# Optimization experiments

Measured on AMD Instinct MI355X. Metric: run time of the kernel, lower is better.

## Reference

```python
import jax, jax.numpy as jnp
import numpy as np
from jax import lax

B, S, IN, H = 16, 128, 200, 256


def _lstm_dir(x_tb, Wih, Whh, bih, bhh):
    # x_tb: [S, B, in]; PyTorch LSTM gate order (i, f, g, o)
    h0 = jnp.zeros((x_tb.shape[1], H), x_tb.dtype)

    def step(carry, x_t):
        h, c = carry
        g = x_t @ Wih.T + h @ Whh.T + bih + bhh  # [B, 4H]
        i, f, gg, o = jnp.split(g, 4, axis=-1)
        c = jax.nn.sigmoid(f) * c + jax.nn.sigmoid(i) * jnp.tanh(gg)
        h = jax.nn.sigmoid(o) * jnp.tanh(c)
        return (h, c), h

    _, hs = lax.scan(step, (h0, h0), x_tb)
    return hs  # [S, B, H]


def _bilstm_layer(x, Wih, Whh, bih, bhh):
    # x: [B, S, in]; params stacked over direction axis [2, ...]
    xt = jnp.swapaxes(x, 0, 1)
    f = _lstm_dir(xt, Wih[0], Whh[0], bih[0], bhh[0])
    b = _lstm_dir(xt[::-1], Wih[1], Whh[1], bih[1], bhh[1])[::-1]
    return jnp.swapaxes(jnp.concatenate([f, b], axis=-1), 0, 1)  # [B, S, 2H]


def _forward(sentence, Wih0, Whh0, bih0, bhh0, Wih1, Whh1, bih1, bhh1,
             W1, b1, W2, b2, W3, b3, tree):
    emb = _bilstm_layer(sentence, Wih0, Whh0, bih0, bhh0)  # [B,S,512]
    emb = _bilstm_layer(emb, Wih1, Whh1, bih1, bhh1)       # [B,S,512]
    D = emb.shape[-1]
    # fc1 on concat(emb[v1], emb[v2]) == per-node halves + broadcast add
    Ha = emb @ W1[:, :D].T   # [B,S,256] head part
    Hb = emb @ W1[:, D:].T   # [B,S,256] dependent part
    h1 = jax.nn.relu(Ha[:, :, None, :] + Hb[:, None, :, :] + b1)  # [B,S,S,256]
    h2 = jax.nn.relu(h1 @ W2.T + b2)                               # [B,S,S,128]
    score = jax.nn.relu(jnp.squeeze(h2 @ W3.T + b3, -1))           # [B,S,S]
    v = jnp.arange(S)
    # valid edges: dep >= 1, head != dep (root col 0 and diagonal stay 0)
    mask = (v[None, :] != v[:, None]) & (v[None, :] >= 1)
    score = score * mask[None, :, :]

    heads, deps = tree[:, 1:, 0], tree[:, 1:, 1]  # [B, S-1]
    K = S - 1
    idx = jnp.broadcast_to(deps[:, None, :], (B, S, K))
    cols = jnp.take_along_axis(score, idx, axis=2)     # score[b, j, dep_k]
    excl = v[None, :, None] == deps[:, None, :]        # exclude j == dep
    norm = jnp.sum(jnp.where(excl, 0.0, jnp.exp(cols)), axis=1)  # [B,K]
    num = score[jnp.arange(B)[:, None], heads, deps]             # [B,K]
    loss = jnp.sum(jnp.sum(jnp.log(norm) - num, axis=-1) / (S - 1))
    return loss, score


def setup_inputs() -> dict:
    key = jax.random.key(0)
    ks = jax.random.split(key, 17)
    sc = jnp.float32(0.05)

    def n(k, shape):
        return jax.random.normal(k, shape, jnp.float32) * sc

    return {
        "sentence": jax.random.normal(ks[0], (B, S, IN), jnp.float32),
        "Wih0": n(ks[1], (2, 4 * H, IN)),
        "Whh0": n(ks[2], (2, 4 * H, H)),
        "bih0": n(ks[3], (2, 4 * H)),
        "bhh0": n(ks[4], (2, 4 * H)),
        "Wih1": n(ks[5], (2, 4 * H, 2 * H)),
        "Whh1": n(ks[6], (2, 4 * H, H)),
        "bih1": n(ks[7], (2, 4 * H)),
        "bhh1": n(ks[8], (2, 4 * H)),
        "W1": n(ks[9], (256, 1024)),
        "b1": n(ks[10], (256,)),
        "W2": n(ks[11], (128, 256)),
        "b2": n(ks[12], (128,)),
        "W3": n(ks[13], (1, 128)),
        "b3": n(ks[14], (1,)),
        "real_dependency_tree": jax.random.randint(ks[15], (B, S, 2), 0, S, jnp.int32),
        "real_seq_len": jnp.full((B,), S, jnp.int32),
    }


def reference(sentence, Wih0, Whh0, bih0, bhh0, Wih1, Whh1, bih1, bhh1,
              W1, b1, W2, b2, W3, b3, real_dependency_tree, real_seq_len):
    # all sentences are full length S (real_seq_len == S), so shapes are static
    del real_seq_len
    return _forward(sentence, Wih0, Whh0, bih0, bhh0, Wih1, Whh1, bih1, bhh1,
                    W1, b1, W2, b2, W3, b3, real_dependency_tree)
```

## Files before the change

kernel.cpp:

```cpp
#include <hip/hip_runtime.h>
#include <hip/hip_bf16.h>
#include <cstdint>
#include <cstddef>


typedef __attribute__((ext_vector_type(8))) short bf16x8;
typedef __attribute__((ext_vector_type(4))) float f32x4;
typedef __attribute__((ext_vector_type(4))) unsigned short u16x4;

__device__ __forceinline__ float bf2f(unsigned short u) {
    return __uint_as_float(((unsigned)u) << 16);
}
__device__ __forceinline__ unsigned short f2bf(float f) {
    unsigned u = __float_as_uint(f);
    u = (u + 0x7FFFu + ((u >> 16) & 1u)) >> 16;
    return (unsigned short)u;
}

__device__ __forceinline__ unsigned f2e4m3(float f) {
    unsigned u = __float_as_uint(f);
    unsigned s = (u >> 24) & 0x80u;
    int expf_ = (int)((u >> 23) & 0xFF);
    if (expf_ == 0) return s;
    int exp = expf_ - 127;
    if (exp < -10) return s;
    unsigned M = (u & 0x7FFFFF) | 0x800000;
    int e8 = exp + 7;
    int shift = 20;
    if (e8 < 1) { shift = 21 - e8; e8 = 0; }
    unsigned q = M >> shift;
    unsigned rem = M & ((1u << shift) - 1u);
    unsigned half = 1u << (shift - 1);
    if (rem > half || (rem == half && (q & 1))) q++;
    if (q >= 16) { q >>= 1; e8++; }
    if (e8 == 0 && (q & 8)) e8 = 1;
    if (e8 >= 16 || (e8 == 15 && (q & 7) == 7)) return s | 0x7Eu;
    return s | ((unsigned)e8 << 4) | (q & 7u);
}


__global__ void k_transpose_N1024(const float* __restrict__ src, float* __restrict__ dst, int K) {
    int z = blockIdx.z;
    int idx = blockIdx.x * 256 + threadIdx.x;
    if (idx >= K * 1024) return;
    int k = idx >> 10, n = idx & 1023;
    dst[(size_t)z * K * 1024 + idx] = src[(size_t)z * 1024 * K + (size_t)n * K + k];
}

__global__ void k_wfrag8(const float* __restrict__ Whh, unsigned char* __restrict__ Wfrag8) {
    int idx = blockIdx.x * 256 + threadIdx.x;
    int l = idx & 63;
    int t = (idx >> 6) & 3;
    int ks = (idx >> 8) & 7;
    int w = (idx >> 11) & 15;
    int d = idx >> 15;
    int r = l & 15;
    int kbase = ks * 32 + (l >> 4) * 8;
    int row = (r & 3) * 256 + w * 16 + t * 4 + (r >> 2);
    const float* src = Whh + (size_t)d * (1024 * 256) + (size_t)row * 256 + kbase;
    unsigned char* dst = Wfrag8 + (size_t)idx * 8;
#pragma unroll
    for (int e = 0; e < 8; ++e) {
        int c = (e & 1) * 4 + (e >> 1);
        dst[e] = (unsigned char)f2e4m3(64.f * src[c]);
    }
}

__global__ void k_w2frag(const float* __restrict__ W2, unsigned short* __restrict__ w2f) {
    int idx = blockIdx.x * 256 + threadIdx.x;
    if (idx >= 4096) return;
    int l = idx & 63;
    int ks = (idx >> 6) & 7;
    int nt = idx >> 9;
    const float* src = W2 + (size_t)(nt * 16 + (l & 15)) * 256 + ks * 32 + (l >> 4) * 8;
    unsigned short* dst = w2f + (size_t)idx * 8;
#pragma unroll
    for (int e = 0; e < 8; ++e) dst[e] = f2bf(src[e]);
}

__global__ void k_w1t(const float* __restrict__ W1, float* __restrict__ dst) {
    int idx = blockIdx.x * 256 + threadIdx.x;
    if (idx >= 512 * 512) return;
    int k = idx >> 9, o = idx & 511;
    dst[idx] = (o < 256) ? W1[(size_t)o * 1024 + k] : W1[(size_t)(o - 256) * 1024 + 512 + k];
}

__global__ void k_bias(const float* __restrict__ bih0, const float* __restrict__ bhh0,
                       const float* __restrict__ bih1, const float* __restrict__ bhh1,
                       const float* __restrict__ b1,
                       float* __restrict__ bsum0, float* __restrict__ bsum1, float* __restrict__ bhab) {
    int idx = blockIdx.x * 256 + threadIdx.x;
    if (idx < 2048) bsum0[idx] = bih0[idx] + bhh0[idx];
    else if (idx < 4096) { int i = idx - 2048; bsum1[i] = bih1[i] + bhh1[i]; }
    else if (idx < 4608) { int i = idx - 4096; bhab[i] = (i < 256) ? b1[i] : 0.f; }
}

__global__ __launch_bounds__(256) void k_reorder(const float* __restrict__ xg, float* __restrict__ xgf) {
    int idx = blockIdx.x * 256 + threadIdx.x;
    int n4 = idx & 255;
    int m = (idx >> 8) & 2047;
    int d = idx >> 19;
    int n0 = n4 * 4;
    int q = n0 >> 8;
    int jbase = n0 & 255;
    int b = m >> 7, t = m & 127;
    float4 v = *(const float4*)(xg + ((size_t)(d * 2048 + m)) * 1024 + n0);
    float* base = xgf + (size_t)d * 2097152;
    float vv[4] = {v.x * 64.f, v.y * 64.f, v.z * 64.f, v.w * 64.f};
#pragma unroll
    for (int dj = 0; dj < 4; ++dj) {
        int j = jbase + dj;
        int fi = (t * 4096 + (j >> 4) * 256 + ((j >> 2) & 3) * 64 + dj * 16 + b) * 4 + q;
        base[fi] = vv[dj];
    }
}

__global__ __launch_bounds__(256) void k_gemm(
    const float* __restrict__ A, const float* __restrict__ Wt,
    const float* __restrict__ bias, float* __restrict__ out,
    int M, int K, int N)
{
    int z = blockIdx.z;
    const float* Wtz = Wt + (size_t)z * K * N;
    float* outz = out + (size_t)z * M * N;
    const float* biasz = bias + (size_t)z * N;

    __shared__ float As[16 * 512];
    int tid = threadIdx.x;
    int mq = tid >> 6;
    int nq = tid & 63;
    int n0 = blockIdx.x * 256 + nq * 4;
    int mbase = blockIdx.y * 16;

    for (int r = 0; r < 16; ++r) {
        const float* Ar = A + (size_t)(mbase + r) * K;
        for (int c = tid; c < K; c += 256) As[r * K + c] = Ar[c];
    }
    __syncthreads();

    float4 bv = *(const float4*)(biasz + n0);
    float acc[4][4];
#pragma unroll
    for (int mi = 0; mi < 4; mi++) { acc[mi][0] = bv.x; acc[mi][1] = bv.y; acc[mi][2] = bv.z; acc[mi][3] = bv.w; }

    const float* asr = As + (mq * 4) * K;
    for (int k = 0; k < K; ++k) {
        float4 w = *(const float4*)(Wtz + (size_t)k * N + n0);
        float x0 = asr[k];
        float x1 = asr[K + k];
        float x2 = asr[2 * K + k];
        float x3 = asr[3 * K + k];
        acc[0][0] += x0 * w.x; acc[0][1] += x0 * w.y; acc[0][2] += x0 * w.z; acc[0][3] += x0 * w.w;
        acc[1][0] += x1 * w.x; acc[1][1] += x1 * w.y; acc[1][2] += x1 * w.z; acc[1][3] += x1 * w.w;
        acc[2][0] += x2 * w.x; acc[2][1] += x2 * w.y; acc[2][2] += x2 * w.z; acc[2][3] += x2 * w.w;
        acc[3][0] += x3 * w.x; acc[3][1] += x3 * w.y; acc[3][2] += x3 * w.z; acc[3][3] += x3 * w.w;
    }
#pragma unroll
    for (int mi = 0; mi < 4; mi++) {
        size_t m = (size_t)mbase + mq * 4 + mi;
        *(float4*)(outz + m * N + n0) = make_float4(acc[mi][0], acc[mi][1], acc[mi][2], acc[mi][3]);
    }
}

__global__ __launch_bounds__(256) void k_gemm_tl(
    const unsigned short* __restrict__ embt, const float* __restrict__ Wt,
    const float* __restrict__ bias, float* __restrict__ out,
    int K, int N)
{
    int z = blockIdx.z;
    const float* Wtz = Wt + (size_t)z * K * N;
    float* outz = out + (size_t)z * 2048 * N;
    const float* biasz = bias + (size_t)z * N;

    __shared__ float As[16 * 512];
    int tid = threadIdx.x;
    int mq = tid >> 6;
    int nq = tid & 63;
    int n0 = blockIdx.x * 256 + nq * 4;
    int mbase = blockIdx.y * 16;
    int bb = mbase >> 7;
    int tt0 = mbase & 127;

    for (int r = 0; r < 16; ++r) {
        const unsigned short* Ar = embt + (size_t)(tt0 + r) * 8192 + bb;
        for (int c = tid; c < K; c += 256) As[r * K + c] = bf2f(Ar[c * 16]);
    }
    __syncthreads();

    float4 bv = *(const float4*)(biasz + n0);
    float acc[4][4];
#pragma unroll
    for (int mi = 0; mi < 4; mi++) { acc[mi][0] = bv.x; acc[mi][1] = bv.y; acc[mi][2] = bv.z; acc[mi][3] = bv.w; }

    const float* asr = As + (mq * 4) * K;
    for (int k = 0; k < K; ++k) {
        float4 w = *(const float4*)(Wtz + (size_t)k * N + n0);
        float x0 = asr[k];
        float x1 = asr[K + k];
        float x2 = asr[2 * K + k];
        float x3 = asr[3 * K + k];
        acc[0][0] += x0 * w.x; acc[0][1] += x0 * w.y; acc[0][2] += x0 * w.z; acc[0][3] += x0 * w.w;
        acc[1][0] += x1 * w.x; acc[1][1] += x1 * w.y; acc[1][2] += x1 * w.z; acc[1][3] += x1 * w.w;
        acc[2][0] += x2 * w.x; acc[2][1] += x2 * w.y; acc[2][2] += x2 * w.z; acc[2][3] += x2 * w.w;
        acc[3][0] += x3 * w.x; acc[3][1] += x3 * w.y; acc[3][2] += x3 * w.z; acc[3][3] += x3 * w.w;
    }
#pragma unroll
    for (int mi = 0; mi < 4; mi++) {
        size_t m = (size_t)mbase + mq * 4 + mi;
        *(float4*)(outz + m * N + n0) = make_float4(acc[mi][0], acc[mi][1], acc[mi][2], acc[mi][3]);
    }
}

#define GATE8(A, C, H) { \
    float gi = A[0] * 0.015625f, gf = A[1] * 0.015625f, gg = A[2] * 0.015625f, go = A[3] * 0.015625f; \
    float si = __builtin_amdgcn_rcpf(1.f + __expf(-gi)); \
    float sf = __builtin_amdgcn_rcpf(1.f + __expf(-gf)); \
    float so = __builtin_amdgcn_rcpf(1.f + __expf(-go)); \
    float eg = __expf(2.f * gg); \
    float tg = 1.f - 2.f * __builtin_amdgcn_rcpf(eg + 1.f); \
    C = sf * C + si * tg; \
    float ec = __expf(2.f * C); \
    float tc = 1.f - 2.f * __builtin_amdgcn_rcpf(ec + 1.f); \
    H = so * tc; }

__global__ __launch_bounds__(512, 2) void k_lstm_mfma(
    const float* __restrict__ xgf,
    const unsigned char* __restrict__ Wfrag8,
    unsigned short* __restrict__ embt)
{
    const int d = blockIdx.x;
    const int tid = threadIdx.x;
    const int wv = tid >> 6;
    const int l = tid & 63;
    const int b = l & 15;
    const int jh = l >> 4;
    const int s0 = wv * 2, s1 = wv * 2 + 1;

    __shared__ __align__(8) unsigned char hB[4096];

    const unsigned char* wg0 = Wfrag8 + ((size_t)(d * 16 + s0)) * 16384;
    const unsigned char* wg1 = Wfrag8 + ((size_t)(d * 16 + s1)) * 16384;
    long W0[8][4], W1[8][4];
#pragma unroll
    for (int ks = 0; ks < 8; ++ks)
#pragma unroll
        for (int t4 = 0; t4 < 4; ++t4) {
            W0[ks][t4] = *(const long*)(wg0 + ((size_t)((ks * 4 + t4) * 64 + l)) * 8);
            W1[ks][t4] = *(const long*)(wg1 + ((size_t)((ks * 4 + t4) * 64 + l)) * 8);
        }
#pragma unroll
    for (int ks = 0; ks < 8; ++ks)
#pragma unroll
        for (int t4 = 0; t4 < 4; ++t4) {
            asm volatile("" : "+v"(W0[ks][t4]));
            asm volatile("" : "+v"(W1[ks][t4]));
        }

    ((uint64_t*)hB)[tid] = 0ull;

    const int sgn = d ? -1 : 1;
    int t = d ? 127 : 0;
    const f32x4* xb = (const f32x4*)(xgf) + (size_t)d * 524288;
    const int xo0 = s0 * 256 + l;
    const int xo1 = s1 * 256 + l;

    f32x4 a0 = xb[t * 4096 + xo0];
    f32x4 a1 = xb[t * 4096 + xo0 + 64];
    f32x4 a2 = xb[t * 4096 + xo0 + 128];
    f32x4 a3 = xb[t * 4096 + xo0 + 192];
    f32x4 e0 = xb[t * 4096 + xo1];
    f32x4 e1 = xb[t * 4096 + xo1 + 64];
    f32x4 e2 = xb[t * 4096 + xo1 + 128];
    f32x4 e3 = xb[t * 4096 + xo1 + 192];

    float c0 = 0.f, c1 = 0.f, c2 = 0.f, c3 = 0.f;
    float c4 = 0.f, c5 = 0.f, c6 = 0.f, c7 = 0.f;
    const int hrd = jh * 128 + b * 8;
    unsigned short* ep0 = embt + (size_t)d * 4096 + (size_t)s0 * 256 + l;
    unsigned short* ep1 = embt + (size_t)d * 4096 + (size_t)s1 * 256 + l;
    unsigned char* hw0 = hB + s0 * 256 + b * 8 + jh * 2;
    unsigned char* hw1 = hB + s1 * 256 + b * 8 + jh * 2;
    __syncthreads();

    for (int s = 0; s < 128; ++s) {
#pragma unroll
        for (int ks = 0; ks < 8; ++ks) {
            long hf = *(const long*)(hB + ks * 512 + hrd);
            a0 = __builtin_amdgcn_mfma_f32_16x16x32_fp8_fp8(W0[ks][0], hf, a0, 0, 0, 0);
            a1 = __builtin_amdgcn_mfma_f32_16x16x32_fp8_fp8(W0[ks][1], hf, a1, 0, 0, 0);
            a2 = __builtin_amdgcn_mfma_f32_16x16x32_fp8_fp8(W0[ks][2], hf, a2, 0, 0, 0);
            a3 = __builtin_amdgcn_mfma_f32_16x16x32_fp8_fp8(W0[ks][3], hf, a3, 0, 0, 0);
            e0 = __builtin_amdgcn_mfma_f32_16x16x32_fp8_fp8(W1[ks][0], hf, e0, 0, 0, 0);
            e1 = __builtin_amdgcn_mfma_f32_16x16x32_fp8_fp8(W1[ks][1], hf, e1, 0, 0, 0);
            e2 = __builtin_amdgcn_mfma_f32_16x16x32_fp8_fp8(W1[ks][2], hf, e2, 0, 0, 0);
            e3 = __builtin_amdgcn_mfma_f32_16x16x32_fp8_fp8(W1[ks][3], hf, e3, 0, 0, 0);
        }

        float h0, h1, h2, h3, h4, h5, h6, h7;
        GATE8(a0, c0, h0);
        GATE8(a1, c1, h1);
        GATE8(a2, c2, h2);
        GATE8(a3, c3, h3);
        GATE8(e0, c4, h4);
        GATE8(e1, c5, h5);
        GATE8(e2, c6, h6);
        GATE8(e3, c7, h7);

        unsigned r01, r23, r45, r67;
        asm("v_cvt_pk_bf16_f32 %0, %1, %2" : "=v"(r01) : "v"(h0), "v"(h1));
        asm("v_cvt_pk_bf16_f32 %0, %1, %2" : "=v"(r23) : "v"(h2), "v"(h3));
        asm("v_cvt_pk_bf16_f32 %0, %1, %2" : "=v"(r45) : "v"(h4), "v"(h5));
        asm("v_cvt_pk_bf16_f32 %0, %1, %2" : "=v"(r67) : "v"(h6), "v"(h7));
        {
            unsigned short* p0 = ep0 + (size_t)t * 8192;
            p0[0]   = (unsigned short)r01;
            p0[64]  = (unsigned short)(r01 >> 16);
            p0[128] = (unsigned short)r23;
            p0[192] = (unsigned short)(r23 >> 16);
            unsigned short* p1 = ep1 + (size_t)t * 8192;
            p1[0]   = (unsigned short)r45;
            p1[64]  = (unsigned short)(r45 >> 16);
            p1[128] = (unsigned short)r67;
            p1[192] = (unsigned short)(r67 >> 16);
        }

        unsigned q01 = __builtin_amdgcn_cvt_pk_fp8_f32(h0, h1, 0, false);
        unsigned q23 = __builtin_amdgcn_cvt_pk_fp8_f32(h2, h3, 0, false);
        unsigned q45 = __builtin_amdgcn_cvt_pk_fp8_f32(h4, h5, 0, false);
        unsigned q67 = __builtin_amdgcn_cvt_pk_fp8_f32(h6, h7, 0, false);

        int tn = (s == 127) ? t : (t + sgn);
        a0 = xb[tn * 4096 + xo0];
        a1 = xb[tn * 4096 + xo0 + 64];
        a2 = xb[tn * 4096 + xo0 + 128];
        a3 = xb[tn * 4096 + xo0 + 192];
        e0 = xb[tn * 4096 + xo1];
        e1 = xb[tn * 4096 + xo1 + 64];
        e2 = xb[tn * 4096 + xo1 + 128];
        e3 = xb[tn * 4096 + xo1 + 192];
        __syncthreads();
        *(unsigned short*)(hw0)       = (unsigned short)q01;
        *(unsigned short*)(hw0 + 128) = (unsigned short)q23;
        *(unsigned short*)(hw1)       = (unsigned short)q45;
        *(unsigned short*)(hw1 + 128) = (unsigned short)q67;
        __syncthreads();
        t = tn;
    }
}

__global__ __launch_bounds__(256, 2) void k_scorer_mfma(
    const float* __restrict__ HaHb, const unsigned short* __restrict__ w2f,
    const float* __restrict__ b2, const float* __restrict__ W3,
    const float* __restrict__ b3v, float* __restrict__ score)
{
    const int jt = blockIdx.x, it = blockIdx.y, b = blockIdx.z;
    const int j0 = jt * 16, i0 = it * 16;
    const int tid = threadIdx.x;
    const int w = tid >> 6;
    const int l = tid & 63;
    const int n_l = l & 15;
    const int kq = l >> 4;

    __shared__ __align__(16) unsigned short HaS[16 * 264];
    __shared__ __align__(16) unsigned short HbS[16 * 264];

    {
        const float* base = HaHb + ((size_t)(b * 128)) * 512;
        int rr = tid >> 4;
        int q = tid & 15;
#pragma unroll
        for (int rep = 0; rep < 4; ++rep) {
            int k0 = q * 4 + rep * 64;
            float4 va = *(const float4*)(base + (size_t)(i0 + rr) * 512 + k0);
            float4 vb = *(const float4*)(base + (size_t)(j0 + rr) * 512 + 256 + k0);
            u16x4 ua = { f2bf(va.x), f2bf(va.y), f2bf(va.z), f2bf(va.w) };
            u16x4 ub = { f2bf(vb.x), f2bf(vb.y), f2bf(vb.z), f2bf(vb.w) };
            *(u16x4*)(&HaS[rr * 264 + k0]) = ua;
            *(u16x4*)(&HbS[rr * 264 + k0]) = ub;
        }
    }

    float b2v[8], w3v[8];
#pragma unroll
    for (int nt = 0; nt < 8; ++nt) {
        b2v[nt] = b2[nt * 16 + n_l];
        w3v[nt] = W3[nt * 16 + n_l];
    }

    f32x4 acc[4][8];
#pragma unroll
    for (int il = 0; il < 4; ++il)
#pragma unroll
        for (int nt = 0; nt < 8; ++nt) acc[il][nt] = f32x4{0.f, 0.f, 0.f, 0.f};

    const bf16x8* wbase = (const bf16x8*)w2f;
    bf16x8 wf[8], wfn[8];
#pragma unroll
    for (int nt = 0; nt < 8; ++nt) wf[nt] = wbase[(nt * 8 + 0) * 64 + l];

    __syncthreads();

#pragma unroll
    for (int ks = 0; ks < 8; ++ks) {
        if (ks < 7) {
#pragma unroll
            for (int nt = 0; nt < 8; ++nt) wfn[nt] = wbase[(nt * 8 + ks + 1) * 64 + l];
        }
#pragma unroll
        for (int il = 0; il < 4; ++il) {
            const int irow = w * 4 + il;
            bf16x8 ha = *(const bf16x8*)(&HaS[irow * 264 + ks * 32 + kq * 8]);
            bf16x8 hb = *(const bf16x8*)(&HbS[n_l * 264 + ks * 32 + kq * 8]);
            bf16x8 av;
#pragma unroll
            for (int e = 0; e < 8; ++e) {
                float v = bf2f((unsigned short)ha[e]) + bf2f((unsigned short)hb[e]);
                v = v > 0.f ? v : 0.f;
                av[e] = (short)f2bf(v);
            }
#pragma unroll
            for (int nt = 0; nt < 8; ++nt)
                acc[il][nt] = __builtin_amdgcn_mfma_f32_16x16x32_bf16(av, wf[nt], acc[il][nt], 0, 0, 0);
        }
#pragma unroll
        for (int nt = 0; nt < 8; ++nt) wf[nt] = wfn[nt];
    }

    const float bb3 = b3v[0];
#pragma unroll
    for (int il = 0; il < 4; ++il) {
        float p[4];
#pragma unroll
        for (int reg = 0; reg < 4; ++reg) {
            float v = 0.f;
#pragma unroll
            for (int nt = 0; nt < 8; ++nt) {
                float h2v = acc[il][nt][reg] + b2v[nt];
                h2v = h2v > 0.f ? h2v : 0.f;
                v += h2v * w3v[nt];
            }
            p[reg] = v;
        }
#pragma unroll
        for (int m = 1; m < 16; m <<= 1) {
            p[0] += __shfl_xor(p[0], m);
            p[1] += __shfl_xor(p[1], m);
            p[2] += __shfl_xor(p[2], m);
            p[3] += __shfl_xor(p[3], m);
        }
        if (n_l == 0) {
            const int i = i0 + w * 4 + il;
            const int jb = j0 + kq * 4;
            float4 sv;
            float* pv = &sv.x;
#pragma unroll
            for (int reg = 0; reg < 4; ++reg) {
                int jg = jb + reg;
                float sc = p[reg] + bb3;
                sc = sc > 0.f ? sc : 0.f;
                if (jg == i || jg == 0) sc = 0.f;
                pv[reg] = sc;
            }
            *(float4*)(&score[((size_t)(b * 128 + i)) * 128 + jb]) = sv;
        }
    }
}

__global__ __launch_bounds__(128) void k_loss1(
    const float* __restrict__ score, const int* __restrict__ tree, float* __restrict__ res)
{
    int k = blockIdx.x;
    int b = blockIdx.y;
    int head = tree[((size_t)b * 128 + k + 1) * 2 + 0];
    int dep  = tree[((size_t)b * 128 + k + 1) * 2 + 1];
    int i = threadIdx.x;
    float s = score[((size_t)b * 128 + i) * 128 + dep];
    float v = (i == dep) ? 0.f : __expf(s);
    __shared__ float redu[2];
#pragma unroll
    for (int off = 32; off >= 1; off >>= 1) v += __shfl_down(v, off, 64);
    if ((i & 63) == 0) redu[i >> 6] = v;
    __syncthreads();
    if (i == 0) {
        float norm = redu[0] + redu[1];
        float num = score[((size_t)b * 128 + head) * 128 + dep];
        res[b * 127 + k] = __logf(norm) - num;
    }
}

__global__ __launch_bounds__(256) void k_loss2(const float* __restrict__ res, float* __restrict__ out) {
    int tid = threadIdx.x;
    float a = 0.f;
    for (int idx = tid; idx < 16 * 127; idx += 256) a += res[idx];
    __shared__ float sm[256];
    sm[tid] = a;
    __syncthreads();
    for (int off = 128; off >= 1; off >>= 1) {
        if (tid < off) sm[tid] += sm[tid + off];
        __syncthreads();
    }
    if (tid == 0) out[0] = sm[0] / 127.f;
}

extern "C" void kernel_launch(void* const* d_in, const int* in_sizes, int n_in,
                              void* d_out, int out_size, void* d_ws, size_t ws_size,
                              hipStream_t stream) {
    (void)in_sizes; (void)n_in; (void)out_size; (void)ws_size;
    const float* X    = (const float*)d_in[0];
    const float* Wih0 = (const float*)d_in[1];
    const float* Whh0 = (const float*)d_in[2];
    const float* bih0 = (const float*)d_in[3];
    const float* bhh0 = (const float*)d_in[4];
    const float* Wih1 = (const float*)d_in[5];
    const float* Whh1 = (const float*)d_in[6];
    const float* bih1 = (const float*)d_in[7];
    const float* bhh1 = (const float*)d_in[8];
    const float* W1   = (const float*)d_in[9];
    const float* b1   = (const float*)d_in[10];
    const float* W2   = (const float*)d_in[11];
    const float* b2   = (const float*)d_in[12];
    const float* W3   = (const float*)d_in[13];
    const float* b3   = (const float*)d_in[14];
    const int*   tree = (const int*)d_in[15];
    float* out = (float*)d_out;

    float* ws = (float*)d_ws;
    size_t o = 0;
    float* WihT0 = ws + o; o += (size_t)2 * 200 * 1024;
    float* WihT1 = ws + o; o += (size_t)2 * 512 * 1024;
    float* W1T   = ws + o; o += (size_t)512 * 512;
    float* bsum0 = ws + o; o += 2048;
    float* bsum1 = ws + o; o += 2048;
    float* bhab  = ws + o; o += 512;
    unsigned char* Wf0 = (unsigned char*)(ws + o); o += (size_t)2 * 16 * 8 * 4 * 64 * 8 / 4;
    unsigned char* Wf1 = (unsigned char*)(ws + o); o += (size_t)2 * 16 * 8 * 4 * 64 * 8 / 4;
    unsigned short* w2f = (unsigned short*)(ws + o); o += (size_t)8 * 8 * 64 * 8 / 2;
    float* xg   = ws + o; o += (size_t)2 * 2048 * 1024;
    float* xgf  = ws + o; o += (size_t)2 * 2048 * 1024;
    unsigned short* embt0 = (unsigned short*)(ws + o); o += (size_t)128 * 512 * 16 / 2;
    unsigned short* embt1 = (unsigned short*)(ws + o); o += (size_t)128 * 512 * 16 / 2;
    float* HaHb = ws + o; o += (size_t)2048 * 512;
    float* res  = ws + o; o += 2048;

    k_transpose_N1024<<<dim3(800, 1, 2), 256, 0, stream>>>(Wih0, WihT0, 200);
    k_transpose_N1024<<<dim3(2048, 1, 2), 256, 0, stream>>>(Wih1, WihT1, 512);
    k_wfrag8<<<256, 256, 0, stream>>>(Whh0, Wf0);
    k_wfrag8<<<256, 256, 0, stream>>>(Whh1, Wf1);
    k_w2frag<<<16, 256, 0, stream>>>(W2, w2f);
    k_w1t<<<1024, 256, 0, stream>>>(W1, W1T);
    k_bias<<<18, 256, 0, stream>>>(bih0, bhh0, bih1, bhh1, b1, bsum0, bsum1, bhab);

    k_gemm<<<dim3(4, 128, 2), 256, 0, stream>>>(X, WihT0, bsum0, xg, 2048, 200, 1024);
    k_reorder<<<4096, 256, 0, stream>>>(xg, xgf);
    k_lstm_mfma<<<2, 512, 0, stream>>>(xgf, Wf0, embt0);
    k_gemm_tl<<<dim3(4, 128, 2), 256, 0, stream>>>(embt0, WihT1, bsum1, xg, 512, 1024);
    k_reorder<<<4096, 256, 0, stream>>>(xg, xgf);
    k_lstm_mfma<<<2, 512, 0, stream>>>(xgf, Wf1, embt1);
    k_gemm_tl<<<dim3(2, 128, 1), 256, 0, stream>>>(embt1, W1T, bhab, HaHb, 512, 512);
    k_scorer_mfma<<<dim3(8, 8, 16), 256, 0, stream>>>(HaHb, w2f, b2, W3, b3, out + 1);
    k_loss1<<<dim3(127, 16), 128, 0, stream>>>(out + 1, tree, res);
    k_loss2<<<1, 256, 0, stream>>>(res, out);
}
```

Measured before the change: 792.2 us.

## Move half of recurrent LSTM weights from registers into LDS

Each wave now keeps only one slice of the fp8 recurrent weights in registers and reads the second slice from a 128KB LDS buffer on every timestep. The slice assignment changes from adjacent pairs (2*wv, 2*wv+1) to wv and wv+8 so the LDS half is contiguous. This halves the register footprint of the weight fragments, lowering register pressure and spills. In exchange it adds four LDS reads per k-step on the serial critical path, and the large LDS allocation limits occupancy below the declared launch bound of two blocks per CU.

Result: slower. 810.4 us (+2.3%).

```diff
diff --git a/kernel.cpp b/kernel.cpp
--- a/kernel.cpp
+++ b/kernel.cpp
@@ -234,29 +234,31 @@
     const int l = tid & 63;
     const int b = l & 15;
     const int jh = l >> 4;
-    const int s0 = wv * 2, s1 = wv * 2 + 1;
-
+    const int s0 = wv;
+    const int s1 = wv + 8;
+
+    __shared__ __align__(16) unsigned char Wlds[131072];
     __shared__ __align__(8) unsigned char hB[4096];
 
+    {
+        const uint4* wsrc = (const uint4*)(Wfrag8 + (size_t)d * 262144 + 131072);
+        uint4* wdst = (uint4*)Wlds;
+        for (int i = tid; i < 8192; i += 512) wdst[i] = wsrc[i];
+    }
+    ((uint64_t*)hB)[tid] = 0ull;
+
     const unsigned char* wg0 = Wfrag8 + ((size_t)(d * 16 + s0)) * 16384;
-    const unsigned char* wg1 = Wfrag8 + ((size_t)(d * 16 + s1)) * 16384;
-    long W0[8][4], W1[8][4];
+    long W0[8][4];
 #pragma unroll
     for (int ks = 0; ks < 8; ++ks)
 #pragma unroll
-        for (int t4 = 0; t4 < 4; ++t4) {
+        for (int t4 = 0; t4 < 4; ++t4)
             W0[ks][t4] = *(const long*)(wg0 + ((size_t)((ks * 4 + t4) * 64 + l)) * 8);
-            W1[ks][t4] = *(const long*)(wg1 + ((size_t)((ks * 4 + t4) * 64 + l)) * 8);
-        }
 #pragma unroll
     for (int ks = 0; ks < 8; ++ks)
 #pragma unroll
-        for (int t4 = 0; t4 < 4; ++t4) {
+        for (int t4 = 0; t4 < 4; ++t4)
             asm volatile("" : "+v"(W0[ks][t4]));
-            asm volatile("" : "+v"(W1[ks][t4]));
-        }
-
-    ((uint64_t*)hB)[tid] = 0ull;
 
     const int sgn = d ? -1 : 1;
     int t = d ? 127 : 0;
@@ -276,6 +278,7 @@
     float c0 = 0.f, c1 = 0.f, c2 = 0.f, c3 = 0.f;
     float c4 = 0.f, c5 = 0.f, c6 = 0.f, c7 = 0.f;
     const int hrd = jh * 128 + b * 8;
+    const unsigned char* WpL = Wlds + (size_t)wv * 16384 + (size_t)l * 8;
     unsigned short* ep0 = embt + (size_t)d * 4096 + (size_t)s0 * 256 + l;
     unsigned short* ep1 = embt + (size_t)d * 4096 + (size_t)s1 * 256 + l;
     unsigned char* hw0 = hB + s0 * 256 + b * 8 + jh * 2;
@@ -286,14 +289,18 @@
 #pragma unroll
         for (int ks = 0; ks < 8; ++ks) {
             long hf = *(const long*)(hB + ks * 512 + hrd);
+            long w0 = *(const long*)(WpL + (ks * 4 + 0) * 512);
+            long w1 = *(const long*)(WpL + (ks * 4 + 1) * 512);
+            long w2 = *(const long*)(WpL + (ks * 4 + 2) * 512);
+            long w3 = *(const long*)(WpL + (ks * 4 + 3) * 512);
             a0 = __builtin_amdgcn_mfma_f32_16x16x32_fp8_fp8(W0[ks][0], hf, a0, 0, 0, 0);
             a1 = __builtin_amdgcn_mfma_f32_16x16x32_fp8_fp8(W0[ks][1], hf, a1, 0, 0, 0);
             a2 = __builtin_amdgcn_mfma_f32_16x16x32_fp8_fp8(W0[ks][2], hf, a2, 0, 0, 0);
             a3 = __builtin_amdgcn_mfma_f32_16x16x32_fp8_fp8(W0[ks][3], hf, a3, 0, 0, 0);
-            e0 = __builtin_amdgcn_mfma_f32_16x16x32_fp8_fp8(W1[ks][0], hf, e0, 0, 0, 0);
-            e1 = __builtin_amdgcn_mfma_f32_16x16x32_fp8_fp8(W1[ks][1], hf, e1, 0, 0, 0);
-            e2 = __builtin_amdgcn_mfma_f32_16x16x32_fp8_fp8(W1[ks][2], hf, e2, 0, 0, 0);
-            e3 = __builtin_amdgcn_mfma_f32_16x16x32_fp8_fp8(W1[ks][3], hf, e3, 0, 0, 0);
+            e0 = __builtin_amdgcn_mfma_f32_16x16x32_fp8_fp8(w0, hf, e0, 0, 0, 0);
+            e1 = __builtin_amdgcn_mfma_f32_16x16x32_fp8_fp8(w1, hf, e1, 0, 0, 0);
+            e2 = __builtin_amdgcn_mfma_f32_16x16x32_fp8_fp8(w2, hf, e2, 0, 0, 0);
+            e3 = __builtin_amdgcn_mfma_f32_16x16x32_fp8_fp8(w3, hf, e3, 0, 0, 0);
         }
 
         float h0, h1, h2, h3, h4, h5, h6, h7;
```

## Replace scalar fp32 layer-1 and fc1 GEMMs with bf16 MFMA GEMM

Applied to the files above, without the earlier changes.

Replaces the scalar FMA GEMMs for the layer-1 input projection and the fc1 head/dependent projection with a bf16 MFMA 16x16x32 kernel. Weights are pre-packed into MFMA B-fragment layout, and a new kernel re-lays the embedding from time-major interleaved layout into row-major bf16 rows for the A operand. The goal is to cut the compute cost of the two largest non-recurrent GEMMs, at the price of extra layout passes and bf16 rounding of the weights.

New measurement: 680.0 us. 14.2% less time.

```diff
diff --git a/kernel.cpp b/kernel.cpp
--- a/kernel.cpp
+++ b/kernel.cpp
@@ -78,11 +78,34 @@
     for (int e = 0; e < 8; ++e) dst[e] = f2bf(src[e]);
 }
 
-__global__ void k_w1t(const float* __restrict__ W1, float* __restrict__ dst) {
-    int idx = blockIdx.x * 256 + threadIdx.x;
-    if (idx >= 512 * 512) return;
-    int k = idx >> 9, o = idx & 511;
-    dst[idx] = (o < 256) ? W1[(size_t)o * 1024 + k] : W1[(size_t)(o - 256) * 1024 + 512 + k];
+__global__ void k_wfragb_ih1(const float* __restrict__ Wih1, unsigned short* __restrict__ wf) {
+    int o = blockIdx.x * 256 + threadIdx.x;
+    int l = o & 63;
+    int nt = (o >> 6) & 63;
+    int ks = (o >> 12) & 15;
+    int z = o >> 16;
+    int n = nt * 16 + (l & 15);
+    int k0 = ks * 32 + (l >> 4) * 8;
+    const float* src = Wih1 + ((size_t)z * 1024 + n) * 512 + k0;
+    unsigned short* dst = wf + (size_t)o * 8;
+#pragma unroll
+    for (int e = 0; e < 8; ++e) dst[e] = f2bf(src[e]);
+}
+
+__global__ void k_wfragb_w1(const float* __restrict__ W1, unsigned short* __restrict__ wf) {
+    int o = blockIdx.x * 256 + threadIdx.x;
+    int l = o & 63;
+    int nt = (o >> 6) & 31;
+    int ks = o >> 11;
+    int oc = nt * 16 + (l & 15);
+    int k0 = ks * 32 + (l >> 4) * 8;
+    unsigned short* dst = wf + (size_t)o * 8;
+#pragma unroll
+    for (int e = 0; e < 8; ++e) {
+        int k = k0 + e;
+        float v = (oc < 256) ? W1[(size_t)oc * 1024 + k] : W1[(size_t)(oc - 256) * 1024 + 512 + k];
+        dst[e] = f2bf(v);
+    }
 }
 
 __global__ void k_bias(const float* __restrict__ bih0, const float* __restrict__ bhh0,
@@ -115,6 +138,18 @@
     }
 }
 
+__global__ __launch_bounds__(256) void k_embR(const unsigned short* __restrict__ embt,
+                                              unsigned short* __restrict__ embR) {
+    int t = blockIdx.x;
+    for (int j = threadIdx.x; j < 512; j += 256) {
+        uint4 v = *(const uint4*)(embt + (size_t)t * 8192 + j * 16);
+        const unsigned short* pv = (const unsigned short*)&v;
+#pragma unroll
+        for (int b = 0; b < 16; ++b)
+            embR[((size_t)(b * 128 + t)) * 512 + j] = pv[b];
+    }
+}
+
 __global__ __launch_bounds__(256) void k_gemm(
     const float* __restrict__ A, const float* __restrict__ Wt,
     const float* __restrict__ bias, float* __restrict__ out,
@@ -162,53 +197,77 @@
     }
 }
 
-__global__ __launch_bounds__(256) void k_gemm_tl(
-    const unsigned short* __restrict__ embt, const float* __restrict__ Wt,
-    const float* __restrict__ bias, float* __restrict__ out,
-    int K, int N)
+__global__ __launch_bounds__(256) void k_mgemm(
+    const unsigned short* __restrict__ embR,
+    const unsigned short* __restrict__ wf,
+    const float* __restrict__ bias,
+    float* __restrict__ out,
+    int N)
 {
-    int z = blockIdx.z;
-    const float* Wtz = Wt + (size_t)z * K * N;
-    float* outz = out + (size_t)z * 2048 * N;
-    const float* biasz = bias + (size_t)z * N;
-
-    __shared__ float As[16 * 512];
-    int tid = threadIdx.x;
-    int mq = tid >> 6;
-    int nq = tid & 63;
-    int n0 = blockIdx.x * 256 + nq * 4;
-    int mbase = blockIdx.y * 16;
-    int bb = mbase >> 7;
-    int tt0 = mbase & 127;
-
-    for (int r = 0; r < 16; ++r) {
-        const unsigned short* Ar = embt + (size_t)(tt0 + r) * 8192 + bb;
-        for (int c = tid; c < K; c += 256) As[r * K + c] = bf2f(Ar[c * 16]);
+    const int z = blockIdx.z;
+    const int NT = N >> 4;
+    const int tid = threadIdx.x;
+    const int w = tid >> 6;
+    const int l = tid & 63;
+    const int arow = l & 15;
+    const int kq = l >> 4;
+    const int mbase = blockIdx.y * 64;
+    const int ntb = blockIdx.x * 16 + w * 4;
+
+    __shared__ __align__(16) unsigned short As[64 * 520];
+
+    for (int i = tid; i < 4096; i += 256) {
+        int r = i >> 6, k8 = i & 63;
+        *(bf16x8*)(&As[r * 520 + k8 * 8]) =
+            *(const bf16x8*)(embR + (size_t)(mbase + r) * 512 + k8 * 8);
+    }
+
+    const bf16x8* wb = (const bf16x8*)wf + (size_t)z * 16 * NT * 64;
+    bf16x8 bf[4], bfn[4];
+#pragma unroll
+    for (int ntl = 0; ntl < 4; ++ntl) bf[ntl] = wb[(size_t)(0 * NT + ntb + ntl) * 64 + l];
+
+    f32x4 acc[4][4];
+#pragma unroll
+    for (int ntl = 0; ntl < 4; ++ntl) {
+        float bv = bias[(size_t)z * N + (ntb + ntl) * 16 + arow];
+#pragma unroll
+        for (int mt = 0; mt < 4; ++mt) acc[mt][ntl] = f32x4{bv, bv, bv, bv};
     }
     __syncthreads();
 
-    float4 bv = *(const float4*)(biasz + n0);
-    float acc[4][4];
-#pragma unroll
-    for (int mi = 0; mi < 4; mi++) { acc[mi][0] = bv.x; acc[mi][1] = bv.y; acc[mi][2] = bv.z; acc[mi][3] = bv.w; }
-
-    const float* asr = As + (mq * 4) * K;
-    for (int k = 0; k < K; ++k) {
-        float4 w = *(const float4*)(Wtz + (size_t)k * N + n0);
-        float x0 = asr[k];
-        float x1 = asr[K + k];
-        float x2 = asr[2 * K + k];
-        float x3 = asr[3 * K + k];
-        acc[0][0] += x0 * w.x; acc[0][1] += x0 * w.y; acc[0][2] += x0 * w.z; acc[0][3] += x0 * w.w;
-        acc[1][0] += x1 * w.x; acc[1][1] += x1 * w.y; acc[1][2] += x1 * w.z; acc[1][3] += x1 * w.w;
-        acc[2][0] += x2 * w.x; acc[2][1] += x2 * w.y; acc[2][2] += x2 * w.z; acc[2][3] += x2 * w.w;
-        acc[3][0] += x3 * w.x; acc[3][1] += x3 * w.y; acc[3][2] += x3 * w.z; acc[3][3] += x3 * w.w;
-    }
-#pragma unroll
-    for (int mi = 0; mi < 4; mi++) {
-        size_t m = (size_t)mbase + mq * 4 + mi;
-        *(float4*)(outz + m * N + n0) = make_float4(acc[mi][0], acc[mi][1], acc[mi][2], acc[mi][3]);
-    }
+#pragma unroll
+    for (int ks = 0; ks < 16; ++ks) {
+        if (ks < 15) {
+#pragma unroll
+            for (int ntl = 0; ntl < 4; ++ntl)
+                bfn[ntl] = wb[(size_t)((ks + 1) * NT + ntb + ntl) * 64 + l];
+        }
+        bf16x8 af[4];
+#pragma unroll
+        for (int mt = 0; mt < 4; ++mt)
+            af[mt] = *(const bf16x8*)(&As[(mt * 16 + arow) * 520 + ks * 32 + kq * 8]);
+#pragma unroll
+        for (int mt = 0; mt < 4; ++mt)
+#pragma unroll
+            for (int ntl = 0; ntl < 4; ++ntl)
+                acc[mt][ntl] = __builtin_amdgcn_mfma_f32_16x16x32_bf16(af[mt], bf[ntl], acc[mt][ntl], 0, 0, 0);
+#pragma unroll
+        for (int ntl = 0; ntl < 4; ++ntl) bf[ntl] = bfn[ntl];
+    }
+
+    float* oz = out + (size_t)z * 2048 * N;
+#pragma unroll
+    for (int mt = 0; mt < 4; ++mt)
+#pragma unroll
+        for (int ntl = 0; ntl < 4; ++ntl) {
+            int ncol = (ntb + ntl) * 16 + arow;
+#pragma unroll
+            for (int reg = 0; reg < 4; ++reg) {
+                int m = mbase + mt * 16 + kq * 4 + reg;
+                oz[(size_t)m * N + ncol] = acc[mt][ntl][reg];
+            }
+        }
 }
 
 #define GATE8(A, C, H) { \
@@ -527,36 +586,39 @@
     float* ws = (float*)d_ws;
     size_t o = 0;
     float* WihT0 = ws + o; o += (size_t)2 * 200 * 1024;
-    float* WihT1 = ws + o; o += (size_t)2 * 512 * 1024;
-    float* W1T   = ws + o; o += (size_t)512 * 512;
     float* bsum0 = ws + o; o += 2048;
     float* bsum1 = ws + o; o += 2048;
     float* bhab  = ws + o; o += 512;
-    unsigned char* Wf0 = (unsigned char*)(ws + o); o += (size_t)2 * 16 * 8 * 4 * 64 * 8 / 4;
-    unsigned char* Wf1 = (unsigned char*)(ws + o); o += (size_t)2 * 16 * 8 * 4 * 64 * 8 / 4;
-    unsigned short* w2f = (unsigned short*)(ws + o); o += (size_t)8 * 8 * 64 * 8 / 2;
+    unsigned char* Wf0 = (unsigned char*)(ws + o); o += (size_t)2 * 16 * 16384 / 4;
+    unsigned char* Wf1 = (unsigned char*)(ws + o); o += (size_t)2 * 16 * 16384 / 4;
+    unsigned short* w2f   = (unsigned short*)(ws + o); o += (size_t)4096 * 8 / 2;
+    unsigned short* wfIh1 = (unsigned short*)(ws + o); o += (size_t)131072 * 8 / 2;
+    unsigned short* wfW1  = (unsigned short*)(ws + o); o += (size_t)32768 * 8 / 2;
     float* xg   = ws + o; o += (size_t)2 * 2048 * 1024;
     float* xgf  = ws + o; o += (size_t)2 * 2048 * 1024;
     unsigned short* embt0 = (unsigned short*)(ws + o); o += (size_t)128 * 512 * 16 / 2;
     unsigned short* embt1 = (unsigned short*)(ws + o); o += (size_t)128 * 512 * 16 / 2;
+    unsigned short* embR  = (unsigned short*)(ws + o); o += (size_t)2048 * 512 / 2;
     float* HaHb = ws + o; o += (size_t)2048 * 512;
     float* res  = ws + o; o += 2048;
 
     k_transpose_N1024<<<dim3(800, 1, 2), 256, 0, stream>>>(Wih0, WihT0, 200);
-    k_transpose_N1024<<<dim3(2048, 1, 2), 256, 0, stream>>>(Wih1, WihT1, 512);
     k_wfrag8<<<256, 256, 0, stream>>>(Whh0, Wf0);
     k_wfrag8<<<256, 256, 0, stream>>>(Whh1, Wf1);
     k_w2frag<<<16, 256, 0, stream>>>(W2, w2f);
-    k_w1t<<<1024, 256, 0, stream>>>(W1, W1T);
+    k_wfragb_ih1<<<512, 256, 0, stream>>>(Wih1, wfIh1);
+    k_wfragb_w1<<<128, 256, 0, stream>>>(W1, wfW1);
     k_bias<<<18, 256, 0, stream>>>(bih0, bhh0, bih1, bhh1, b1, bsum0, bsum1, bhab);
 
     k_gemm<<<dim3(4, 128, 2), 256, 0, stream>>>(X, WihT0, bsum0, xg, 2048, 200, 1024);
     k_reorder<<<4096, 256, 0, stream>>>(xg, xgf);
     k_lstm_mfma<<<2, 512, 0, stream>>>(xgf, Wf0, embt0);
-    k_gemm_tl<<<dim3(4, 128, 2), 256, 0, stream>>>(embt0, WihT1, bsum1, xg, 512, 1024);
+    k_embR<<<128, 256, 0, stream>>>(embt0, embR);
+    k_mgemm<<<dim3(4, 32, 2), 256, 0, stream>>>(embR, wfIh1, bsum1, xg, 1024);
     k_reorder<<<4096, 256, 0, stream>>>(xg, xgf);
     k_lstm_mfma<<<2, 512, 0, stream>>>(xgf, Wf1, embt1);
-    k_gemm_tl<<<dim3(2, 128, 1), 256, 0, stream>>>(embt1, W1T, bhab, HaHb, 512, 512);
+    k_embR<<<128, 256, 0, stream>>>(embt1, embR);
+    k_mgemm<<<dim3(2, 32, 1), 256, 0, stream>>>(embR, wfW1, bhab, HaHb, 512);
     k_scorer_mfma<<<dim3(8, 8, 16), 256, 0, stream>>>(HaHb, w2f, b2, W3, b3, out + 1);
     k_loss1<<<dim3(127, 16), 128, 0, stream>>>(out + 1, tree, res);
     k_loss2<<<1, 256, 0, stream>>>(res, out);
```
